# Kernel optimization log

Hardware: AMD Instinct MI355X
Metric: run time of the kernel (lower is better)

The kernel has to match this reference:

```python
import jax, jax.numpy as jnp
import numpy as np

N_NODES = 500000
N_EDGES = 16000000
IN_DIM = 17


def setup_inputs() -> dict:
    key = jax.random.key(0)
    k1, k2, k3, k4, k5, k6, k7 = jax.random.split(key, 7)
    x = jax.random.normal(k1, (N_NODES, IN_DIM), dtype=jnp.float32)
    edge_index = jax.random.randint(k2, (2, N_EDGES), 0, N_NODES, dtype=jnp.int64)
    edge_weight = jax.random.uniform(k3, (N_EDGES,), dtype=jnp.float32)
    # SAGEConv(17, 1): lin_l applied to aggregated neighbors (with bias),
    # lin_r applied to root features (no bias, PyG convention).
    s = 1.0 / np.sqrt(IN_DIM)
    w_l = jax.random.uniform(k4, (1, IN_DIM), minval=-s, maxval=s, dtype=jnp.float32)
    b_l = jax.random.uniform(k5, (1,), minval=-s, maxval=s, dtype=jnp.float32)
    w_r = jax.random.uniform(k6, (1, IN_DIM), minval=-s, maxval=s, dtype=jnp.float32)
    # out: Linear(1, 1)
    k8, k9 = jax.random.split(k7)
    w_o = jax.random.uniform(k8, (1, 1), minval=-1.0, maxval=1.0, dtype=jnp.float32)
    b_o = jax.random.uniform(k9, (1,), minval=-1.0, maxval=1.0, dtype=jnp.float32)
    return {"x": x, "edge_index": edge_index, "edge_weight": edge_weight,
            "w_l": w_l, "b_l": b_l, "w_r": w_r, "w_o": w_o, "b_o": b_o}


def reference(x, edge_index, edge_weight, w_l, b_l, w_r, w_o, b_o):
    # SAGEConv (mean aggregation). edge_weight is unused (faithful to PyG SAGEConv).
    # Project to out_dim=1 BEFORE aggregation (linearity makes this exact and
    # avoids materializing a [E,17] gathered buffer):
    #   lin_l(mean_j x_j) + b_l == mean_j (x_j @ W_l^T) + b_l
    src, dst = edge_index[0], edge_index[1]
    x_proj_l = x @ w_l.T                      # [N, 1]
    msg = x_proj_l[src, 0]                    # [E]  gathered source projections
    agg = jax.ops.segment_sum(msg, dst, num_segments=x.shape[0])          # [N]
    cnt = jax.ops.segment_sum(jnp.ones_like(msg), dst, num_segments=x.shape[0])
    mean = agg / jnp.maximum(cnt, 1.0)        # zero for isolated nodes
    h = mean[:, None] + b_l + x @ w_r.T       # [N, 1]  lin_l(aggr) + lin_r(x)
    h = jax.nn.elu(h)
    return h @ w_o.T + b_o                    # [N, 1]
```

## Files before the change

kernel.cpp:

```cpp
#include <hip/hip_runtime.h>
#include <hip/hip_bf16.h>
#include <math.h>

#define IN_DIM 17
#define NB 128
#define LOG_BN 12
#define BN 4096
#define K_SPLIT 8
#define CHUNK 8192
#define EPT 32
#define VAL_SCALE 4096.0f
#define FP_SCALE 268435456.0f
#define FP_INV   (1.0 / 268435456.0)

__global__ void node_proj_kernel(const float* __restrict__ x,
                                 const float* __restrict__ w_l,
                                 const float* __restrict__ w_r,
                                 float* __restrict__ p_l,
                                 float* __restrict__ p_r,
                                 int n_nodes) {
    int i = blockIdx.x * blockDim.x + threadIdx.x;
    if (i >= n_nodes) return;
    const float* row = x + (size_t)i * IN_DIM;
    float sl = 0.0f, sr = 0.0f;
#pragma unroll
    for (int k = 0; k < IN_DIM; ++k) {
        float v = row[k];
        sl = fmaf(v, w_l[k], sl);
        sr = fmaf(v, w_r[k], sr);
    }
    p_l[i] = sl;
    p_r[i] = sr;
}

__global__ __launch_bounds__(256, 4)
void sort_scatter_kernel(const int* __restrict__ src,
                         const int* __restrict__ dst,
                         const float* __restrict__ p_l,
                         unsigned* __restrict__ staging,
                         unsigned short* __restrict__ segtab,
                         int n_edges) {
    __shared__ unsigned hist[NB];
    __shared__ unsigned cnt[NB];
    __shared__ unsigned scanbuf[NB];
    __shared__ unsigned sstart[NB + 1];
    __shared__ unsigned lbuf[CHUNK];

    const int tid = threadIdx.x;
    const int blk = blockIdx.x;
    const int e0 = blk * CHUNK;
    const int chunk_n = min(CHUNK, n_edges - e0);
    const int nvec = chunk_n >> 2;

    for (int t = tid; t < NB; t += 256) { hist[t] = 0; cnt[t] = 0; }
    __syncthreads();

    uint4 dreg[EPT / 4];
    const uint4* dv = (const uint4*)(dst + e0);
#pragma unroll
    for (int k = 0; k < EPT / 4; ++k) {
        int q = tid + k * 256;
        if (q < nvec) {
            uint4 d = dv[q];
            dreg[k] = d;
            atomicAdd(&hist[d.x >> LOG_BN], 1u);
            atomicAdd(&hist[d.y >> LOG_BN], 1u);
            atomicAdd(&hist[d.z >> LOG_BN], 1u);
            atomicAdd(&hist[d.w >> LOG_BN], 1u);
        }
    }
    for (int i = (nvec << 2) + tid; i < chunk_n; i += 256)
        atomicAdd(&hist[(unsigned)dst[e0 + i] >> LOG_BN], 1u);
    __syncthreads();

    if (tid < NB) scanbuf[tid] = hist[tid];
    __syncthreads();
    for (int off = 1; off < NB; off <<= 1) {
        unsigned v = 0;
        if (tid < NB && tid >= off) v = scanbuf[tid - off];
        __syncthreads();
        if (tid < NB && tid >= off) scanbuf[tid] += v;
        __syncthreads();
    }
    if (tid < NB) sstart[tid + 1] = scanbuf[tid];
    if (tid == 0) sstart[0] = 0;
    __syncthreads();

    for (int t = tid; t <= NB; t += 256)
        segtab[(size_t)blk * (NB + 2) + t] = (unsigned short)sstart[t];

    const uint4* sv = (const uint4*)(src + e0);
#pragma unroll
    for (int k = 0; k < EPT / 4; ++k) {
        int q = tid + k * 256;
        if (q < nvec) {
            uint4 s = sv[q];
            uint4 d = dreg[k];
            float p0 = p_l[s.x], p1 = p_l[s.y], p2 = p_l[s.z], p3 = p_l[s.w];
            unsigned pp[4], dd[4] = {d.x, d.y, d.z, d.w};
            float pf[4] = {p0, p1, p2, p3};
#pragma unroll
            for (int u = 0; u < 4; ++u) {
                int fx = __float2int_rn(pf[u] * VAL_SCALE);
                fx = max(-32768, min(32767, fx));
                pp[u] = ((unsigned)(fx & 0xFFFF) << 16) | (dd[u] & (BN - 1));
            }
#pragma unroll
            for (int u = 0; u < 4; ++u) {
                unsigned b = dd[u] >> LOG_BN;
                unsigned pos = sstart[b] + atomicAdd(&cnt[b], 1u);
                lbuf[pos] = pp[u];
            }
        }
    }
    for (int i = (nvec << 2) + tid; i < chunk_n; i += 256) {
        unsigned s = (unsigned)src[e0 + i];
        unsigned d = (unsigned)dst[e0 + i];
        int fx = __float2int_rn(p_l[s] * VAL_SCALE);
        fx = max(-32768, min(32767, fx));
        unsigned entry = ((unsigned)(fx & 0xFFFF) << 16) | (d & (BN - 1));
        unsigned b = d >> LOG_BN;
        unsigned pos = sstart[b] + atomicAdd(&cnt[b], 1u);
        lbuf[pos] = entry;
    }
    __syncthreads();

    uint4* outp = (uint4*)(staging + (size_t)blk * CHUNK);
    const uint4* lp = (const uint4*)lbuf;
    int nv4 = (chunk_n + 3) >> 2;
    for (int q = tid; q < nv4; q += 256)
        outp[q] = lp[q];
}

__global__ __launch_bounds__(256, 4)
void reduce_kernel(const unsigned* __restrict__ staging,
                   const unsigned short* __restrict__ segtab,
                   unsigned* __restrict__ partials,
                   int nblk) {
    __shared__ unsigned lds_p[BN];
    const int tid = threadIdx.x;
    const int b = blockIdx.x / K_SPLIT;
    const int j = blockIdx.x % K_SPLIT;
    const int wave = tid >> 6, lane = tid & 63;

    for (int i = tid; i < BN; i += 256) lds_p[i] = 0u;
    __syncthreads();

    const int blk0 = (int)((long long)nblk * j / K_SPLIT);
    const int blk1 = (int)((long long)nblk * (j + 1) / K_SPLIT);

    int blk = blk0 + wave;
    unsigned s_nxt = 0, e_nxt = 0;
    if (blk < blk1) {
        const unsigned short* st = segtab + (size_t)blk * (NB + 2) + b;
        s_nxt = st[0];
        e_nxt = st[1];
    }
    while (blk < blk1) {
        unsigned s = s_nxt, e = e_nxt;
        const int nxt = blk + 4;
        if (nxt < blk1) {
            const unsigned short* st = segtab + (size_t)nxt * (NB + 2) + b;
            s_nxt = st[0];
            e_nxt = st[1];
        }
        const unsigned* sp = staging + (size_t)blk * CHUNK;
        for (unsigned i = s + lane; i < e; i += 64) {
            unsigned en = sp[i];
            int v = (int)(short)(en >> 16);
            atomicAdd(&lds_p[en & (BN - 1)], ((unsigned)v << 8) | 1u);
        }
        blk = nxt;
    }
    __syncthreads();
    size_t out_base = (size_t)blockIdx.x * BN;
    for (int i = tid; i < BN; i += 256)
        partials[out_base + i] = lds_p[i];
}

__global__ void finalize_kernel(const float* __restrict__ p_r,
                                const unsigned* __restrict__ partials,
                                const float* __restrict__ b_l,
                                const float* __restrict__ w_o,
                                const float* __restrict__ b_o,
                                float* __restrict__ out,
                                int n_nodes) {
    int i = blockIdx.x * blockDim.x + threadIdx.x;
    if (i >= n_nodes) return;
    int b = i >> LOG_BN;
    int loc = i & (BN - 1);
    int sum24 = 0, cnt = 0;
#pragma unroll
    for (int j = 0; j < K_SPLIT; ++j) {
        unsigned u = partials[((size_t)b * K_SPLIT + j) * BN + loc];
        sum24 += ((int)u) >> 8;
        cnt += (int)(u & 0xFFu);
    }
    float sum = (float)sum24 * (1.0f / VAL_SCALE);
    float mean = sum / fmaxf((float)cnt, 1.0f);
    float h = mean + b_l[0] + p_r[i];
    h = (h > 0.0f) ? h : expm1f(h);
    out[i] = fmaf(h, w_o[0], b_o[0]);
}

__global__ void edge_scatter_fb(const int* __restrict__ edge_index,
                                const float* __restrict__ p_l,
                                unsigned long long* __restrict__ bins,
                                int n_edges) {
    int e = blockIdx.x * blockDim.x + threadIdx.x;
    if (e >= n_edges) return;
    int s = edge_index[e];
    int d = edge_index[n_edges + e];
    float p = p_l[s];
    long long sfx = (long long)llrintf(p * FP_SCALE);
    unsigned long long delta = ((unsigned long long)sfx << 20) | 1ULL;
    atomicAdd(&bins[d], delta);
}

__global__ void finalize_fb(const float* __restrict__ p_r,
                            const unsigned long long* __restrict__ bins,
                            const float* __restrict__ b_l,
                            const float* __restrict__ w_o,
                            const float* __restrict__ b_o,
                            float* __restrict__ out,
                            int n_nodes) {
    int i = blockIdx.x * blockDim.x + threadIdx.x;
    if (i >= n_nodes) return;
    long long packed = (long long)bins[i];
    int cntv = (int)(packed & 0xFFFFFLL);
    long long sfx = packed >> 20;
    float sum = (float)((double)sfx * FP_INV);
    float mean = sum / fmaxf((float)cntv, 1.0f);
    float h = mean + b_l[0] + p_r[i];
    h = (h > 0.0f) ? h : expm1f(h);
    out[i] = fmaf(h, w_o[0], b_o[0]);
}

static inline size_t align_up(size_t v, size_t a) { return (v + a - 1) & ~(a - 1); }

extern "C" void kernel_launch(void* const* d_in, const int* in_sizes, int n_in,
                              void* d_out, int out_size, void* d_ws, size_t ws_size,
                              hipStream_t stream) {
    const float* x   = (const float*)d_in[0];
    const int*   ei  = (const int*)d_in[1];
    const float* w_l = (const float*)d_in[3];
    const float* b_l = (const float*)d_in[4];
    const float* w_r = (const float*)d_in[5];
    const float* w_o = (const float*)d_in[6];
    const float* b_o = (const float*)d_in[7];
    float* out = (float*)d_out;

    const int n_nodes = in_sizes[0] / IN_DIM;
    const int n_edges = in_sizes[2];
    const int* src = ei;
    const int* dst = ei + n_edges;
    const int nblk = (n_edges + CHUNK - 1) / CHUNK;

    char* ws = (char*)d_ws;
    size_t off = 0;
    size_t o_pl = off;      off = align_up(off + (size_t)n_nodes * 4, 256);
    size_t o_pr = off;      off = align_up(off + (size_t)n_nodes * 4, 256);
    size_t o_stage = off;   off = align_up(off + (size_t)nblk * CHUNK * 4, 256);
    size_t o_seg = off;     off = align_up(off + (size_t)nblk * (NB + 2) * 2, 256);
    size_t o_part = off;    off = align_up(off + (size_t)NB * K_SPLIT * BN * 4, 256);
    size_t need = off;

    float* p_l = (float*)(ws + o_pl);
    float* p_r = (float*)(ws + o_pr);

    const int B = 256;
    node_proj_kernel<<<(n_nodes + B - 1) / B, B, 0, stream>>>(x, w_l, w_r, p_l, p_r, n_nodes);

    if (ws_size >= need) {
        unsigned* staging       = (unsigned*)(ws + o_stage);
        unsigned short* segtab  = (unsigned short*)(ws + o_seg);
        unsigned* partials      = (unsigned*)(ws + o_part);

        sort_scatter_kernel<<<nblk, B, 0, stream>>>(src, dst, p_l, staging, segtab, n_edges);
        reduce_kernel<<<NB * K_SPLIT, B, 0, stream>>>(staging, segtab, partials, nblk);
        finalize_kernel<<<(n_nodes + B - 1) / B, B, 0, stream>>>(p_r, partials, b_l, w_o, b_o,
                                                                 out, n_nodes);
    } else {
        unsigned long long* bins = (unsigned long long*)(ws + o_stage);
        hipMemsetAsync(bins, 0, (size_t)n_nodes * 8, stream);
        edge_scatter_fb<<<(n_edges + B - 1) / B, B, 0, stream>>>(ei, p_l, bins, n_edges);
        finalize_fb<<<(n_nodes + B - 1) / B, B, 0, stream>>>(p_r, bins, b_l, w_o, b_o,
                                                             out, n_nodes);
    }
}
```

Measured before the change: 369.6 us.

## Capture bucket ranks during histogram, use wave-shuffle scan, raise reduce split

```diff
diff --git a/kernel.cpp b/kernel.cpp
--- a/kernel.cpp
+++ b/kernel.cpp
@@ -6,7 +6,7 @@
 #define NB 128
 #define LOG_BN 12
 #define BN 4096
-#define K_SPLIT 8
+#define K_SPLIT 16
 #define CHUNK 8192
 #define EPT 32
 #define VAL_SCALE 4096.0f
@@ -40,9 +40,7 @@
                          unsigned* __restrict__ staging,
                          unsigned short* __restrict__ segtab,
                          int n_edges) {
-    __shared__ unsigned hist[NB];
     __shared__ unsigned cnt[NB];
-    __shared__ unsigned scanbuf[NB];
     __shared__ unsigned sstart[NB + 1];
     __shared__ unsigned lbuf[CHUNK];
 
@@ -52,76 +50,92 @@
     const int chunk_n = min(CHUNK, n_edges - e0);
     const int nvec = chunk_n >> 2;
 
-    for (int t = tid; t < NB; t += 256) { hist[t] = 0; cnt[t] = 0; }
+    for (int t = tid; t < NB; t += 256) cnt[t] = 0;
     __syncthreads();
 
     uint4 dreg[EPT / 4];
+    uint4 sreg[EPT / 4];
+    unsigned rpack[EPT / 2];
     const uint4* dv = (const uint4*)(dst + e0);
+    const uint4* sv = (const uint4*)(src + e0);
 #pragma unroll
     for (int k = 0; k < EPT / 4; ++k) {
         int q = tid + k * 256;
         if (q < nvec) {
             uint4 d = dv[q];
             dreg[k] = d;
-            atomicAdd(&hist[d.x >> LOG_BN], 1u);
-            atomicAdd(&hist[d.y >> LOG_BN], 1u);
-            atomicAdd(&hist[d.z >> LOG_BN], 1u);
-            atomicAdd(&hist[d.w >> LOG_BN], 1u);
-        }
-    }
-    for (int i = (nvec << 2) + tid; i < chunk_n; i += 256)
-        atomicAdd(&hist[(unsigned)dst[e0 + i] >> LOG_BN], 1u);
-    __syncthreads();
-
-    if (tid < NB) scanbuf[tid] = hist[tid];
-    __syncthreads();
-    for (int off = 1; off < NB; off <<= 1) {
-        unsigned v = 0;
-        if (tid < NB && tid >= off) v = scanbuf[tid - off];
-        __syncthreads();
-        if (tid < NB && tid >= off) scanbuf[tid] += v;
-        __syncthreads();
-    }
-    if (tid < NB) sstart[tid + 1] = scanbuf[tid];
-    if (tid == 0) sstart[0] = 0;
+            sreg[k] = sv[q];
+            unsigned r0 = atomicAdd(&cnt[d.x >> LOG_BN], 1u);
+            unsigned r1 = atomicAdd(&cnt[d.y >> LOG_BN], 1u);
+            unsigned r2 = atomicAdd(&cnt[d.z >> LOG_BN], 1u);
+            unsigned r3 = atomicAdd(&cnt[d.w >> LOG_BN], 1u);
+            rpack[2 * k]     = r0 | (r1 << 16);
+            rpack[2 * k + 1] = r2 | (r3 << 16);
+        }
+    }
+    unsigned tail_rank = 0;
+    {
+        int i = (nvec << 2) + tid;
+        if (i < chunk_n)
+            tail_rank = atomicAdd(&cnt[(unsigned)dst[e0 + i] >> LOG_BN], 1u);
+    }
+    __syncthreads();
+
+    if (tid < 64) {
+        unsigned c0 = cnt[tid], c1 = cnt[tid + 64];
+        unsigned s0 = c0;
+#pragma unroll
+        for (int off = 1; off < 64; off <<= 1) {
+            unsigned v = __shfl_up(s0, off);
+            if (tid >= off) s0 += v;
+        }
+        unsigned tot0 = __shfl(s0, 63);
+        unsigned s1 = c1;
+#pragma unroll
+        for (int off = 1; off < 64; off <<= 1) {
+            unsigned v = __shfl_up(s1, off);
+            if (tid >= off) s1 += v;
+        }
+        s1 += tot0;
+        sstart[tid + 1] = s0;
+        sstart[tid + 65] = s1;
+        if (tid == 0) sstart[0] = 0;
+    }
     __syncthreads();
 
     for (int t = tid; t <= NB; t += 256)
         segtab[(size_t)blk * (NB + 2) + t] = (unsigned short)sstart[t];
 
-    const uint4* sv = (const uint4*)(src + e0);
 #pragma unroll
     for (int k = 0; k < EPT / 4; ++k) {
         int q = tid + k * 256;
         if (q < nvec) {
-            uint4 s = sv[q];
+            uint4 s = sreg[k];
             uint4 d = dreg[k];
-            float p0 = p_l[s.x], p1 = p_l[s.y], p2 = p_l[s.z], p3 = p_l[s.w];
-            unsigned pp[4], dd[4] = {d.x, d.y, d.z, d.w};
-            float pf[4] = {p0, p1, p2, p3};
+            float pf[4] = {p_l[s.x], p_l[s.y], p_l[s.z], p_l[s.w]};
+            unsigned dd[4] = {d.x, d.y, d.z, d.w};
+            unsigned rk[4] = {rpack[2 * k] & 0xFFFFu, rpack[2 * k] >> 16,
+                              rpack[2 * k + 1] & 0xFFFFu, rpack[2 * k + 1] >> 16};
 #pragma unroll
             for (int u = 0; u < 4; ++u) {
                 int fx = __float2int_rn(pf[u] * VAL_SCALE);
                 fx = max(-32768, min(32767, fx));
-                pp[u] = ((unsigned)(fx & 0xFFFF) << 16) | (dd[u] & (BN - 1));
+                unsigned entry = ((unsigned)(fx & 0xFFFF) << 16) | (dd[u] & (BN - 1));
+                unsigned b = dd[u] >> LOG_BN;
+                lbuf[sstart[b] + rk[u]] = entry;
             }
-#pragma unroll
-            for (int u = 0; u < 4; ++u) {
-                unsigned b = dd[u] >> LOG_BN;
-                unsigned pos = sstart[b] + atomicAdd(&cnt[b], 1u);
-                lbuf[pos] = pp[u];
-            }
-        }
-    }
-    for (int i = (nvec << 2) + tid; i < chunk_n; i += 256) {
-        unsigned s = (unsigned)src[e0 + i];
-        unsigned d = (unsigned)dst[e0 + i];
-        int fx = __float2int_rn(p_l[s] * VAL_SCALE);
-        fx = max(-32768, min(32767, fx));
-        unsigned entry = ((unsigned)(fx & 0xFFFF) << 16) | (d & (BN - 1));
-        unsigned b = d >> LOG_BN;
-        unsigned pos = sstart[b] + atomicAdd(&cnt[b], 1u);
-        lbuf[pos] = entry;
+        }
+    }
+    {
+        int i = (nvec << 2) + tid;
+        if (i < chunk_n) {
+            unsigned s = (unsigned)src[e0 + i];
+            unsigned d = (unsigned)dst[e0 + i];
+            int fx = __float2int_rn(p_l[s] * VAL_SCALE);
+            fx = max(-32768, min(32767, fx));
+            unsigned entry = ((unsigned)(fx & 0xFFFF) << 16) | (d & (BN - 1));
+            lbuf[sstart[d >> LOG_BN] + tail_rank] = entry;
+        }
     }
     __syncthreads();
 
@@ -132,7 +146,7 @@
         outp[q] = lp[q];
 }
 
-__global__ __launch_bounds__(256, 4)
+__global__ __launch_bounds__(256, 8)
 void reduce_kernel(const unsigned* __restrict__ staging,
                    const unsigned short* __restrict__ segtab,
                    unsigned* __restrict__ partials,
```

Result: faster. 343.1 us (-7.2%).
